# Kernel optimization log

Hardware: AMD Instinct MI355X
Metric: run time of the kernel (lower is better)

## Reference

```python
import jax, jax.numpy as jnp
import numpy as np

N_QUBITS = 4
DEPTH = 3
OUT_DIM = 256
BN_EPS = 1e-5


def _apply_ry(state, theta, q):
    # state: (B,2,2,2,2) complex64, theta: (B,) float32, gate on qubit q
    st = jnp.moveaxis(state, q + 1, -1)            # (B,2,2,2,2) with target last
    half = theta * 0.5
    c = jnp.cos(half)[:, None, None, None]
    s = jnp.sin(half)[:, None, None, None]
    a0, a1 = st[..., 0], st[..., 1]
    st = jnp.stack([c * a0 - s * a1, s * a0 + c * a1], axis=-1)
    return jnp.moveaxis(st, -1, q + 1)


def _apply_rz(state, theta, q):
    # theta: scalar (shared param). RZ = diag(e^{-i t/2}, e^{i t/2})
    st = jnp.moveaxis(state, q + 1, -1)
    p0 = jnp.exp(-0.5j * theta)
    p1 = jnp.exp(0.5j * theta)
    st = jnp.stack([st[..., 0] * p0, st[..., 1] * p1], axis=-1)
    return jnp.moveaxis(st, -1, q + 1)


def _apply_cnot(state, c, t):
    st = jnp.moveaxis(state, (c + 1, t + 1), (-2, -1))  # (...,2_c,2_t)
    st = jnp.stack([st[..., 0, :], st[..., 1, ::-1]], axis=-2)
    return jnp.moveaxis(st, (-2, -1), (c + 1, t + 1))


def _simulate(qparams, x):
    # Batched 4-qubit statevector sim. x: (B,4) data angles, qparams: (24,)
    B = x.shape[0]
    state = jnp.zeros((B, 16), jnp.complex64).at[:, 0].set(1.0)
    state = state.reshape(B, 2, 2, 2, 2)
    for d in range(DEPTH):
        for i in range(N_QUBITS):
            # RY(data) then RY(param) on same wire == RY(data+param)
            state = _apply_ry(state, x[:, i] + qparams[d * 2 * N_QUBITS + i], i)
        for i in range(N_QUBITS):
            state = _apply_cnot(state, i, (i + 1) % N_QUBITS)
        for i in range(N_QUBITS):
            theta = qparams[d * 2 * N_QUBITS + N_QUBITS + i]
            state = _apply_rz(state, jnp.broadcast_to(theta, ()), i)
    probs = jnp.abs(state) ** 2                      # (B,2,2,2,2) float32
    axes = (1, 2, 3, 4)
    z = []
    for i in range(N_QUBITS):
        p = probs.sum(axis=tuple(a for a in axes if a != i + 1))  # (B,2)
        z.append(p[:, 0] - p[:, 1])
    return jnp.stack(z, axis=1).astype(jnp.float32)  # (B,4) <Z_i>


def _batchnorm(h, g, b):
    m = h.mean(axis=0)
    v = h.var(axis=0)  # biased, as torch uses for normalization in train mode
    return (h - m) * jax.lax.rsqrt(v + BN_EPS) * g + b


def setup_inputs() -> dict:
    key = jax.random.key(0)
    ks = jax.random.split(key, 8)
    B = 65536
    x = jax.random.normal(ks[0], (B, N_QUBITS), jnp.float32)
    qparams = jax.random.normal(ks[1], (DEPTH * 2 * N_QUBITS,), jnp.float32)
    fc1_w = jax.random.normal(ks[2], (128, N_QUBITS), jnp.float32) * 0.3
    fc1_b = jnp.zeros((128,), jnp.float32)
    fc2_w = jax.random.normal(ks[3], (256, 128), jnp.float32) * 0.08
    fc2_b = jnp.zeros((256,), jnp.float32)
    fc3_w = jax.random.normal(ks[4], (OUT_DIM, 256), jnp.float32) * 0.06
    fc3_b = jnp.zeros((OUT_DIM,), jnp.float32)
    bn1_g = jnp.ones((128,), jnp.float32)
    bn1_b = jnp.zeros((128,), jnp.float32)
    bn2_g = jnp.ones((256,), jnp.float32)
    bn2_b = jnp.zeros((256,), jnp.float32)
    return dict(x=x, qparams=qparams, fc1_w=fc1_w, fc1_b=fc1_b,
                bn1_g=bn1_g, bn1_b=bn1_b, fc2_w=fc2_w, fc2_b=fc2_b,
                bn2_g=bn2_g, bn2_b=bn2_b, fc3_w=fc3_w, fc3_b=fc3_b)


def reference(x, qparams, fc1_w, fc1_b, bn1_g, bn1_b, fc2_w, fc2_b,
              bn2_g, bn2_b, fc3_w, fc3_b):
    q = _simulate(qparams, x)                              # (B,4)
    h = jax.nn.relu(_batchnorm(q @ fc1_w.T + fc1_b, bn1_g, bn1_b))
    h = jax.nn.relu(_batchnorm(h @ fc2_w.T + fc2_b, bn2_g, bn2_b))
    out = jnp.tanh(h @ fc3_w.T + fc3_b)                    # (B,256)
    return out.reshape(-1, 1, 16, 16)
```

## Files before the change

### kernel.cpp

```cpp
#include <hip/hip_runtime.h>

typedef __attribute__((ext_vector_type(8))) _Float16 f16x8;
typedef __attribute__((ext_vector_type(16))) float f32x16;

#define MFMA32(a, b, c) __builtin_amdgcn_mfma_f32_32x32x16_f16((a), (b), (c), 0, 0, 0)

__device__ __forceinline__ float tanh_fast(float x) {
  return 1.0f - 2.0f / (__expf(2.0f * x) + 1.0f);
}

__global__ __launch_bounds__(256) void k_quantum(
    const float4* __restrict__ x, const float* __restrict__ qp,
    float4* __restrict__ qout, float* __restrict__ stats, int QB,
    const float* __restrict__ w2, const float* __restrict__ w3,
    _Float16* __restrict__ w2f, _Float16* __restrict__ w3f)
{
  int tid = threadIdx.x;

  if (blockIdx.x >= QB) {
    int i = (blockIdx.x - QB) * 256 + tid;
    w3f[i] = (_Float16)w3[i];
    if (i < 32768) w2f[i] = (_Float16)w2[i];
    return;
  }

  size_t r = (size_t)blockIdx.x * 256 + tid;
  float4 xr = x[r];
  float xv[4] = {xr.x, xr.y, xr.z, xr.w};

  float re[16], im[16];
#pragma unroll
  for (int i = 0; i < 16; i++) { re[i] = 0.f; im[i] = 0.f; }
  re[0] = 1.f;

#pragma unroll
  for (int d = 0; d < 3; d++) {
#pragma unroll
    for (int q = 0; q < 4; q++) {
      float th = 0.5f * (xv[q] + qp[d * 8 + q]);
      float s, c; __sincosf(th, &s, &c);
      int m = 8 >> q;
#pragma unroll
      for (int i = 0; i < 16; i++) if (!(i & m)) {
        int i1 = i | m;
        float r0 = re[i], i0 = im[i], r1 = re[i1], i1v = im[i1];
        re[i]  = c * r0 - s * r1;  im[i]  = c * i0 - s * i1v;
        re[i1] = s * r0 + c * r1;  im[i1] = s * i0 + c * i1v;
      }
    }
#pragma unroll
    for (int q = 0; q < 4; q++) {
      int mc = 8 >> q, mt = 8 >> ((q + 1) & 3);
#pragma unroll
      for (int i = 0; i < 16; i++) if ((i & mc) && !(i & mt)) {
        int i1 = i | mt;
        float tr = re[i]; re[i] = re[i1]; re[i1] = tr;
        float ti = im[i]; im[i] = im[i1]; im[i1] = ti;
      }
    }
#pragma unroll
    for (int q = 0; q < 4; q++) {
      float th = 0.5f * qp[d * 8 + 4 + q];
      float s, c; __sincosf(th, &s, &c);
      int m = 8 >> q;
#pragma unroll
      for (int i = 0; i < 16; i++) {
        float pi = (i & m) ? s : -s;
        float r0 = re[i], i0 = im[i];
        re[i] = r0 * c - i0 * pi;
        im[i] = r0 * pi + i0 * c;
      }
    }
  }

  float p[16];
#pragma unroll
  for (int i = 0; i < 16; i++) p[i] = re[i] * re[i] + im[i] * im[i];
  float z[4];
#pragma unroll
  for (int q = 0; q < 4; q++) {
    int m = 8 >> q; float acc = 0.f;
#pragma unroll
    for (int i = 0; i < 16; i++) acc += (i & m) ? -p[i] : p[i];
    z[q] = acc;
  }
  qout[r] = make_float4(z[0], z[1], z[2], z[3]);

  float st[14];
  st[0] = z[0]; st[1] = z[1]; st[2] = z[2]; st[3] = z[3];
  int p5 = 4;
#pragma unroll
  for (int a = 0; a < 4; a++)
#pragma unroll
    for (int b = a; b < 4; b++) st[p5++] = z[a] * z[b];

  __shared__ float part[4][14];
  int lane = tid & 63, wv = tid >> 6;
#pragma unroll
  for (int s = 0; s < 14; s++) {
    float v = st[s];
#pragma unroll
    for (int o = 32; o; o >>= 1) v += __shfl_down(v, o, 64);
    if (lane == 0) part[wv][s] = v;
  }
  __syncthreads();
  if (tid < 14)
    atomicAdd(stats + tid, part[0][tid] + part[1][tid] + part[2][tid] + part[3][tid]);
}

__global__ void k_prep1(const float* __restrict__ w1, const float* __restrict__ b1,
                        const float* __restrict__ g, const float* __restrict__ bb,
                        const float* __restrict__ stats, float* __restrict__ w1e,
                        float* __restrict__ b1e, float invB)
{
  int j = threadIdx.x;
  float qb0 = stats[0] * invB, qb1 = stats[1] * invB, qb2 = stats[2] * invB, qb3 = stats[3] * invB;
  float M00 = stats[4] * invB, M01 = stats[5] * invB, M02 = stats[6] * invB, M03 = stats[7] * invB;
  float M11 = stats[8] * invB, M12 = stats[9] * invB, M13 = stats[10] * invB;
  float M22 = stats[11] * invB, M23 = stats[12] * invB, M33 = stats[13] * invB;
  float w0 = w1[j * 4 + 0], wv1 = w1[j * 4 + 1], wv2 = w1[j * 4 + 2], wv3 = w1[j * 4 + 3];
  float b = b1[j];
  float wq = w0 * qb0 + wv1 * qb1 + wv2 * qb2 + wv3 * qb3;
  float m = wq + b;
  float quad = w0 * w0 * M00 + wv1 * wv1 * M11 + wv2 * wv2 * M22 + wv3 * wv3 * M33
             + 2.f * (w0 * wv1 * M01 + w0 * wv2 * M02 + w0 * wv3 * M03
                    + wv1 * wv2 * M12 + wv1 * wv3 * M13 + wv2 * wv3 * M23);
  float e2 = quad + 2.f * b * wq + b * b;
  float var = e2 - m * m;
  float s = g[j] * rsqrtf(var + 1e-5f);
  w1e[j * 4 + 0] = s * w0; w1e[j * 4 + 1] = s * wv1;
  w1e[j * 4 + 2] = s * wv2; w1e[j * 4 + 3] = s * wv3;
  b1e[j] = s * b + bb[j] - s * m;
}

__global__ __launch_bounds__(256, 2) void k_fc2stats(
    const float4* __restrict__ q, const float4* __restrict__ w1e4,
    const float* __restrict__ b1e, const _Float16* __restrict__ w2f,
    const float* __restrict__ b2,
    float* __restrict__ s2sum, float* __restrict__ s2sq)
{
  __shared__ __align__(16) float4 qs[128];
  __shared__ __align__(16) _Float16 a1[128 * 136];

  int t = threadIdx.x;
  int lane = t & 63, w = t >> 6, m32 = lane & 31, hh = lane >> 5;
  size_t rowBase = (size_t)blockIdx.x * 128;

  if (t < 128) qs[t] = q[rowBase + t];
  __syncthreads();

  {
    int j = t & 127;
    float4 w1 = w1e4[j];
    float b1v = b1e[j];
    int rb = (t >> 7) * 64;
#pragma unroll 8
    for (int i = 0; i < 64; i++) {
      float4 qv = qs[rb + i];
      float v = fmaf(w1.x, qv.x, fmaf(w1.y, qv.y, fmaf(w1.z, qv.z, fmaf(w1.w, qv.w, b1v))));
      a1[(rb + i) * 136 + j] = (_Float16)fmaxf(v, 0.f);
    }
  }
  __syncthreads();

  f32x16 acc[4][2];
#pragma unroll
  for (int mt = 0; mt < 4; mt++)
#pragma unroll
    for (int nt = 0; nt < 2; nt++)
#pragma unroll
      for (int r = 0; r < 16; r++) acc[mt][nt][r] = 0.f;

#pragma unroll
  for (int ks = 0; ks < 8; ks++) {
    int kb = ks * 16 + hh * 8;
    f16x8 bfr[2];
#pragma unroll
    for (int nt = 0; nt < 2; nt++)
      bfr[nt] = *(const f16x8*)(w2f + (size_t)(w * 64 + nt * 32 + m32) * 128 + kb);
#pragma unroll
    for (int mt = 0; mt < 4; mt++) {
      f16x8 afr = *(const f16x8*)&a1[(mt * 32 + m32) * 136 + kb];
#pragma unroll
      for (int nt = 0; nt < 2; nt++)
        acc[mt][nt] = MFMA32(afr, bfr[nt], acc[mt][nt]);
    }
  }

#pragma unroll
  for (int nt = 0; nt < 2; nt++) {
    int col = w * 64 + nt * 32 + m32;
    float b2v = b2[col];
    float s = 0.f, ss = 0.f;
#pragma unroll
    for (int mt = 0; mt < 4; mt++)
#pragma unroll
      for (int r = 0; r < 16; r++) {
        float hv = acc[mt][nt][r] + b2v;
        s += hv; ss += hv * hv;
      }
    s += __shfl_down(s, 32, 64);
    ss += __shfl_down(ss, 32, 64);
    if (lane < 32) {
      atomicAdd(&s2sum[col], s);
      atomicAdd(&s2sq[col], ss);
    }
  }
}

__global__ void k_prep2(const float* __restrict__ g, const float* __restrict__ bb,
                        const float* __restrict__ b2,
                        const float* __restrict__ s2sum, const float* __restrict__ s2sq,
                        float* __restrict__ sc2, float* __restrict__ t2, float invB)
{
  int j = threadIdx.x;
  float m = s2sum[j] * invB;
  float v = s2sq[j] * invB - m * m;
  float s = g[j] * rsqrtf(v + 1e-5f);
  sc2[j] = s;
  t2[j] = bb[j] - m * s + b2[j] * s;
}

__global__ __launch_bounds__(256, 2) void k_final(
    const float4* __restrict__ q, const float4* __restrict__ w1e4,
    const float* __restrict__ b1e, const _Float16* __restrict__ w2f,
    const float* __restrict__ sc2, const float* __restrict__ t2g,
    const _Float16* __restrict__ w3f, const float* __restrict__ b3,
    float* __restrict__ out)
{
  __shared__ __align__(16) float4 qs[128];
  __shared__ __align__(16) _Float16 un[128 * 264];
  _Float16* a1 = un;
  _Float16* a2 = un;

  int t = threadIdx.x;
  int lane = t & 63, w = t >> 6, m32 = lane & 31, hh = lane >> 5;
  size_t rowBase = (size_t)blockIdx.x * 128;

  if (t < 128) qs[t] = q[rowBase + t];
  __syncthreads();

  {
    int j = t & 127;
    float4 w1 = w1e4[j];
    float b1v = b1e[j];
    int rb = (t >> 7) * 64;
#pragma unroll 8
    for (int i = 0; i < 64; i++) {
      float4 qv = qs[rb + i];
      float v = fmaf(w1.x, qv.x, fmaf(w1.y, qv.y, fmaf(w1.z, qv.z, fmaf(w1.w, qv.w, b1v))));
      a1[(rb + i) * 136 + j] = (_Float16)fmaxf(v, 0.f);
    }
  }
  __syncthreads();

  f32x16 acc[4][2];
#pragma unroll
  for (int mt = 0; mt < 4; mt++)
#pragma unroll
    for (int nt = 0; nt < 2; nt++)
#pragma unroll
      for (int r = 0; r < 16; r++) acc[mt][nt][r] = 0.f;

#pragma unroll
  for (int ks = 0; ks < 8; ks++) {
    int kb = ks * 16 + hh * 8;
    f16x8 bfr[2];
#pragma unroll
    for (int nt = 0; nt < 2; nt++)
      bfr[nt] = *(const f16x8*)(w2f + (size_t)(w * 64 + nt * 32 + m32) * 128 + kb);
#pragma unroll
    for (int mt = 0; mt < 4; mt++) {
      f16x8 afr = *(const f16x8*)&a1[(mt * 32 + m32) * 136 + kb];
#pragma unroll
      for (int nt = 0; nt < 2; nt++)
        acc[mt][nt] = MFMA32(afr, bfr[nt], acc[mt][nt]);
    }
  }
  __syncthreads();

#pragma unroll
  for (int nt = 0; nt < 2; nt++) {
    int col = w * 64 + nt * 32 + m32;
    float sv = sc2[col], tv = t2g[col];
#pragma unroll
    for (int mt = 0; mt < 4; mt++)
#pragma unroll
      for (int r = 0; r < 16; r++) {
        int row = mt * 32 + (r & 3) + 8 * (r >> 2) + 4 * hh;
        a2[row * 264 + col] = (_Float16)fmaxf(fmaf(acc[mt][nt][r], sv, tv), 0.f);
      }
  }
  __syncthreads();

  f32x16 acc3[4][2];
#pragma unroll
  for (int mt = 0; mt < 4; mt++)
#pragma unroll
    for (int nt = 0; nt < 2; nt++)
#pragma unroll
      for (int r = 0; r < 16; r++) acc3[mt][nt][r] = 0.f;

#pragma unroll
  for (int ks = 0; ks < 16; ks++) {
    int kb = ks * 16 + hh * 8;
    f16x8 bfr[2];
#pragma unroll
    for (int nt = 0; nt < 2; nt++)
      bfr[nt] = *(const f16x8*)(w3f + (size_t)(w * 64 + nt * 32 + m32) * 256 + kb);
#pragma unroll
    for (int mt = 0; mt < 4; mt++) {
      f16x8 afr = *(const f16x8*)&a2[(mt * 32 + m32) * 264 + kb];
#pragma unroll
      for (int nt = 0; nt < 2; nt++)
        acc3[mt][nt] = MFMA32(afr, bfr[nt], acc3[mt][nt]);
    }
  }

#pragma unroll
  for (int nt = 0; nt < 2; nt++) {
    int col = w * 64 + nt * 32 + m32;
    float b3v = b3[col];
#pragma unroll
    for (int mt = 0; mt < 4; mt++)
#pragma unroll
      for (int r = 0; r < 16; r++) {
        int row = mt * 32 + (r & 3) + 8 * (r >> 2) + 4 * hh;
        out[(rowBase + row) * 256 + col] = tanh_fast(acc3[mt][nt][r] + b3v);
      }
  }
}

extern "C" void kernel_launch(void* const* d_in, const int* in_sizes, int n_in,
                              void* d_out, int out_size, void* d_ws, size_t ws_size,
                              hipStream_t stream) {
  const float* x     = (const float*)d_in[0];
  const float* qp    = (const float*)d_in[1];
  const float* fc1_w = (const float*)d_in[2];
  const float* fc1_b = (const float*)d_in[3];
  const float* bn1_g = (const float*)d_in[4];
  const float* bn1_b = (const float*)d_in[5];
  const float* fc2_w = (const float*)d_in[6];
  const float* fc2_b = (const float*)d_in[7];
  const float* bn2_g = (const float*)d_in[8];
  const float* bn2_b = (const float*)d_in[9];
  const float* fc3_w = (const float*)d_in[10];
  const float* fc3_b = (const float*)d_in[11];
  float* out = (float*)d_out;
  float* ws  = (float*)d_ws;

  int B = in_sizes[0] / 4;
  int QB = B / 256;

  float* wq    = ws;
  float* s1    = ws + (size_t)4 * B;
  float* w1e   = s1 + 16;
  float* b1e   = w1e + 512;
  float* s2sum = b1e + 128;
  float* s2sq  = s2sum + 256;
  float* sc2   = s2sq + 256;
  float* t2    = sc2 + 256;
  _Float16* w2f = (_Float16*)(t2 + 256);
  _Float16* w3f = w2f + 32768;

  hipMemsetAsync((void*)s1, 0, (16 + 512 + 128 + 256 + 256) * sizeof(float), stream);

  float invB = 1.0f / (float)B;

  k_quantum<<<QB + 256, 256, 0, stream>>>((const float4*)x, qp, (float4*)wq, s1, QB,
                                          fc2_w, fc3_w, w2f, w3f);
  k_prep1<<<1, 128, 0, stream>>>(fc1_w, fc1_b, bn1_g, bn1_b, s1, w1e, b1e, invB);
  k_fc2stats<<<B / 128, 256, 0, stream>>>((const float4*)wq, (const float4*)w1e, b1e,
                                          w2f, fc2_b, s2sum, s2sq);
  k_prep2<<<1, 256, 0, stream>>>(bn2_g, bn2_b, fc2_b, s2sum, s2sq, sc2, t2, invB);
  k_final<<<B / 128, 256, 0, stream>>>((const float4*)wq, (const float4*)w1e, b1e,
                                       w2f, sc2, t2, w3f, fc3_b, out);
}
```

Baseline: 149.0 us.

## Store fc2 activations in fp16 and skip recomputing fc1/fc2 in final kernel

```diff
diff --git a/kernel.cpp b/kernel.cpp
--- a/kernel.cpp
+++ b/kernel.cpp
@@ -133,14 +133,16 @@
   b1e[j] = s * b + bb[j] - s * m;
 }
 
-__global__ __launch_bounds__(256, 2) void k_fc2stats(
+__global__ __launch_bounds__(256, 2) void k_fc2h(
     const float4* __restrict__ q, const float4* __restrict__ w1e4,
     const float* __restrict__ b1e, const _Float16* __restrict__ w2f,
-    const float* __restrict__ b2,
+    const float* __restrict__ b2, _Float16* __restrict__ h2f,
     float* __restrict__ s2sum, float* __restrict__ s2sq)
 {
   __shared__ __align__(16) float4 qs[128];
-  __shared__ __align__(16) _Float16 a1[128 * 136];
+  __shared__ __align__(16) _Float16 un[128 * 260];
+  _Float16* a1 = un;
+  _Float16* h2 = un;
 
   int t = threadIdx.x;
   int lane = t & 63, w = t >> 6, m32 = lane & 31, hh = lane >> 5;
@@ -158,7 +160,7 @@
     for (int i = 0; i < 64; i++) {
       float4 qv = qs[rb + i];
       float v = fmaf(w1.x, qv.x, fmaf(w1.y, qv.y, fmaf(w1.z, qv.z, fmaf(w1.w, qv.w, b1v))));
-      a1[(rb + i) * 136 + j] = (_Float16)fmaxf(v, 0.f);
+      a1[(rb + i) * 132 + j] = (_Float16)fmaxf(v, 0.f);
     }
   }
   __syncthreads();
@@ -180,7 +182,7 @@
       bfr[nt] = *(const f16x8*)(w2f + (size_t)(w * 64 + nt * 32 + m32) * 128 + kb);
 #pragma unroll
     for (int mt = 0; mt < 4; mt++) {
-      f16x8 afr = *(const f16x8*)&a1[(mt * 32 + m32) * 136 + kb];
+      f16x8 afr = *(const f16x8*)&a1[(mt * 32 + m32) * 132 + kb];
 #pragma unroll
       for (int nt = 0; nt < 2; nt++)
         acc[mt][nt] = MFMA32(afr, bfr[nt], acc[mt][nt]);
@@ -206,114 +208,83 @@
       atomicAdd(&s2sq[col], ss);
     }
   }
+  __syncthreads();
+
+#pragma unroll
+  for (int nt = 0; nt < 2; nt++) {
+    int col = w * 64 + nt * 32 + m32;
+#pragma unroll
+    for (int mt = 0; mt < 4; mt++)
+#pragma unroll
+      for (int r = 0; r < 16; r++) {
+        int row = mt * 32 + (r & 3) + 8 * (r >> 2) + 4 * hh;
+        h2[row * 260 + col] = (_Float16)acc[mt][nt][r];
+      }
+  }
+  __syncthreads();
+
+  {
+#pragma unroll
+    for (int i = 0; i < 16; i++) {
+      int idx8 = i * 256 + t;
+      int row = idx8 >> 5;
+      int cik = idx8 & 31;
+      *(uint4*)(h2f + (rowBase + row) * 256 + cik * 8) =
+          *(const uint4*)(h2 + row * 260 + cik * 8);
+    }
+  }
 }
 
 __global__ void k_prep2(const float* __restrict__ g, const float* __restrict__ bb,
                         const float* __restrict__ b2,
                         const float* __restrict__ s2sum, const float* __restrict__ s2sq,
-                        float* __restrict__ sc2, float* __restrict__ t2, float invB)
+                        _Float16* __restrict__ sc2h, _Float16* __restrict__ t2h, float invB)
 {
   int j = threadIdx.x;
   float m = s2sum[j] * invB;
   float v = s2sq[j] * invB - m * m;
   float s = g[j] * rsqrtf(v + 1e-5f);
-  sc2[j] = s;
-  t2[j] = bb[j] - m * s + b2[j] * s;
-}
-
-__global__ __launch_bounds__(256, 2) void k_final(
-    const float4* __restrict__ q, const float4* __restrict__ w1e4,
-    const float* __restrict__ b1e, const _Float16* __restrict__ w2f,
-    const float* __restrict__ sc2, const float* __restrict__ t2g,
+  sc2h[j] = (_Float16)s;
+  t2h[j] = (_Float16)(bb[j] - m * s + b2[j] * s);
+}
+
+__global__ __launch_bounds__(256) void k_fc3(
+    const _Float16* __restrict__ h2f,
+    const _Float16* __restrict__ sc2h, const _Float16* __restrict__ t2h,
     const _Float16* __restrict__ w3f, const float* __restrict__ b3,
     float* __restrict__ out)
 {
-  __shared__ __align__(16) float4 qs[128];
-  __shared__ __align__(16) _Float16 un[128 * 264];
-  _Float16* a1 = un;
-  _Float16* a2 = un;
-
   int t = threadIdx.x;
   int lane = t & 63, w = t >> 6, m32 = lane & 31, hh = lane >> 5;
   size_t rowBase = (size_t)blockIdx.x * 128;
 
-  if (t < 128) qs[t] = q[rowBase + t];
-  __syncthreads();
-
-  {
-    int j = t & 127;
-    float4 w1 = w1e4[j];
-    float b1v = b1e[j];
-    int rb = (t >> 7) * 64;
-#pragma unroll 8
-    for (int i = 0; i < 64; i++) {
-      float4 qv = qs[rb + i];
-      float v = fmaf(w1.x, qv.x, fmaf(w1.y, qv.y, fmaf(w1.z, qv.z, fmaf(w1.w, qv.w, b1v))));
-      a1[(rb + i) * 136 + j] = (_Float16)fmaxf(v, 0.f);
-    }
-  }
-  __syncthreads();
-
-  f32x16 acc[4][2];
+  f32x16 acc3[4][2];
 #pragma unroll
   for (int mt = 0; mt < 4; mt++)
 #pragma unroll
     for (int nt = 0; nt < 2; nt++)
 #pragma unroll
-      for (int r = 0; r < 16; r++) acc[mt][nt][r] = 0.f;
-
-#pragma unroll
-  for (int ks = 0; ks < 8; ks++) {
-    int kb = ks * 16 + hh * 8;
-    f16x8 bfr[2];
-#pragma unroll
-    for (int nt = 0; nt < 2; nt++)
-      bfr[nt] = *(const f16x8*)(w2f + (size_t)(w * 64 + nt * 32 + m32) * 128 + kb);
-#pragma unroll
-    for (int mt = 0; mt < 4; mt++) {
-      f16x8 afr = *(const f16x8*)&a1[(mt * 32 + m32) * 136 + kb];
-#pragma unroll
-      for (int nt = 0; nt < 2; nt++)
-        acc[mt][nt] = MFMA32(afr, bfr[nt], acc[mt][nt]);
-    }
-  }
-  __syncthreads();
-
-#pragma unroll
-  for (int nt = 0; nt < 2; nt++) {
-    int col = w * 64 + nt * 32 + m32;
-    float sv = sc2[col], tv = t2g[col];
-#pragma unroll
-    for (int mt = 0; mt < 4; mt++)
-#pragma unroll
-      for (int r = 0; r < 16; r++) {
-        int row = mt * 32 + (r & 3) + 8 * (r >> 2) + 4 * hh;
-        a2[row * 264 + col] = (_Float16)fmaxf(fmaf(acc[mt][nt][r], sv, tv), 0.f);
-      }
-  }
-  __syncthreads();
-
-  f32x16 acc3[4][2];
-#pragma unroll
-  for (int mt = 0; mt < 4; mt++)
-#pragma unroll
-    for (int nt = 0; nt < 2; nt++)
-#pragma unroll
       for (int r = 0; r < 16; r++) acc3[mt][nt][r] = 0.f;
 
-#pragma unroll
+#pragma unroll 4
   for (int ks = 0; ks < 16; ks++) {
     int kb = ks * 16 + hh * 8;
+    f16x8 sv8 = *(const f16x8*)(sc2h + kb);
+    f16x8 tv8 = *(const f16x8*)(t2h + kb);
     f16x8 bfr[2];
 #pragma unroll
     for (int nt = 0; nt < 2; nt++)
       bfr[nt] = *(const f16x8*)(w3f + (size_t)(w * 64 + nt * 32 + m32) * 256 + kb);
 #pragma unroll
     for (int mt = 0; mt < 4; mt++) {
-      f16x8 afr = *(const f16x8*)&a2[(mt * 32 + m32) * 264 + kb];
+      f16x8 hraw = *(const f16x8*)(h2f + (rowBase + mt * 32 + m32) * 256 + kb);
+      f16x8 af = hraw * sv8 + tv8;
+#pragma unroll
+      for (int j = 0; j < 8; j++)
+        af[j] = (af[j] > (_Float16)0.f) ? af[j] : (_Float16)0.f;
 #pragma unroll
       for (int nt = 0; nt < 2; nt++)
-        acc3[mt][nt] = MFMA32(afr, bfr[nt], acc3[mt][nt]);
+        acc3[mt][nt] = MFMA32(af, bfr[nt], acc3[mt][nt]);
     }
   }
 
@@ -358,10 +329,11 @@
   float* b1e   = w1e + 512;
   float* s2sum = b1e + 128;
   float* s2sq  = s2sum + 256;
-  float* sc2   = s2sq + 256;
-  float* t2    = sc2 + 256;
-  _Float16* w2f = (_Float16*)(t2 + 256);
-  _Float16* w3f = w2f + 32768;
+  _Float16* sc2h = (_Float16*)(s2sq + 256);
+  _Float16* t2h  = sc2h + 256;
+  _Float16* w2f  = t2h + 256;
+  _Float16* w3f  = w2f + 32768;
+  _Float16* h2f  = w3f + 65536;
 
   hipMemsetAsync((void*)s1, 0, (16 + 512 + 128 + 256 + 256) * sizeof(float), stream);
 
@@ -370,9 +342,8 @@
   k_quantum<<<QB + 256, 256, 0, stream>>>((const float4*)x, qp, (float4*)wq, s1, QB,
                                           fc2_w, fc3_w, w2f, w3f);
   k_prep1<<<1, 128, 0, stream>>>(fc1_w, fc1_b, bn1_g, bn1_b, s1, w1e, b1e, invB);
-  k_fc2stats<<<B / 128, 256, 0, stream>>>((const float4*)wq, (const float4*)w1e, b1e,
-                                          w2f, fc2_b, s2sum, s2sq);
-  k_prep2<<<1, 256, 0, stream>>>(bn2_g, bn2_b, fc2_b, s2sum, s2sq, sc2, t2, invB);
-  k_final<<<B / 128, 256, 0, stream>>>((const float4*)wq, (const float4*)w1e, b1e,
-                                       w2f, sc2, t2, w3f, fc3_b, out);
-}
+  k_fc2h<<<B / 128, 256, 0, stream>>>((const float4*)wq, (const float4*)w1e, b1e,
+                                      w2f, fc2_b, h2f, s2sum, s2sq);
+  k_prep2<<<1, 256, 0, stream>>>(bn2_g, bn2_b, fc2_b, s2sum, s2sq, sc2h, t2h, invB);
+  k_fc3<<<B / 128, 256, 0, stream>>>(h2f, sc2h, t2h, w3f, fc3_b, out);
+}
```

New measurement: 183.1 us. +22.9%, slower.

## Halve row tile to 64, pre-block fp16 weights for coalesced loads, shrink memset

Applied to the files above, without the earlier changes.

```diff
diff --git a/kernel.cpp b/kernel.cpp
--- a/kernel.cpp
+++ b/kernel.cpp
@@ -13,14 +13,20 @@
     const float4* __restrict__ x, const float* __restrict__ qp,
     float4* __restrict__ qout, float* __restrict__ stats, int QB,
     const float* __restrict__ w2, const float* __restrict__ w3,
-    _Float16* __restrict__ w2f, _Float16* __restrict__ w3f)
+    _Float16* __restrict__ w2t, _Float16* __restrict__ w3t)
 {
   int tid = threadIdx.x;
 
   if (blockIdx.x >= QB) {
     int i = (blockIdx.x - QB) * 256 + tid;
-    w3f[i] = (_Float16)w3[i];
-    if (i < 32768) w2f[i] = (_Float16)w2[i];
+    {
+      int col = i >> 8, k = i & 255;
+      w3t[((k >> 3) * 256 + col) * 8 + (k & 7)] = (_Float16)w3[i];
+    }
+    if (i < 32768) {
+      int col = i >> 7, k = i & 127;
+      w2t[((k >> 3) * 256 + col) * 8 + (k & 7)] = (_Float16)w2[i];
+    }
     return;
   }
 
@@ -133,39 +139,39 @@
   b1e[j] = s * b + bb[j] - s * m;
 }
 
-__global__ __launch_bounds__(256, 2) void k_fc2stats(
+__global__ __launch_bounds__(256, 4) void k_fc2stats(
     const float4* __restrict__ q, const float4* __restrict__ w1e4,
-    const float* __restrict__ b1e, const _Float16* __restrict__ w2f,
+    const float* __restrict__ b1e, const _Float16* __restrict__ w2t,
     const float* __restrict__ b2,
     float* __restrict__ s2sum, float* __restrict__ s2sq)
 {
-  __shared__ __align__(16) float4 qs[128];
-  __shared__ __align__(16) _Float16 a1[128 * 136];
+  __shared__ __align__(16) float4 qs[64];
+  __shared__ __align__(16) _Float16 a1[64 * 132];
 
   int t = threadIdx.x;
   int lane = t & 63, w = t >> 6, m32 = lane & 31, hh = lane >> 5;
-  size_t rowBase = (size_t)blockIdx.x * 128;
-
-  if (t < 128) qs[t] = q[rowBase + t];
+  size_t rowBase = (size_t)blockIdx.x * 64;
+
+  if (t < 64) qs[t] = q[rowBase + t];
   __syncthreads();
 
   {
     int j = t & 127;
     float4 w1 = w1e4[j];
     float b1v = b1e[j];
-    int rb = (t >> 7) * 64;
+    int rb = (t >> 7) * 32;
 #pragma unroll 8
-    for (int i = 0; i < 64; i++) {
+    for (int i = 0; i < 32; i++) {
       float4 qv = qs[rb + i];
       float v = fmaf(w1.x, qv.x, fmaf(w1.y, qv.y, fmaf(w1.z, qv.z, fmaf(w1.w, qv.w, b1v))));
-      a1[(rb + i) * 136 + j] = (_Float16)fmaxf(v, 0.f);
-    }
-  }
-  __syncthreads();
-
-  f32x16 acc[4][2];
-#pragma unroll
-  for (int mt = 0; mt < 4; mt++)
+      a1[(rb + i) * 132 + j] = (_Float16)fmaxf(v, 0.f);
+    }
+  }
+  __syncthreads();
+
+  f32x16 acc[2][2];
+#pragma unroll
+  for (int mt = 0; mt < 2; mt++)
 #pragma unroll
     for (int nt = 0; nt < 2; nt++)
 #pragma unroll
@@ -174,13 +180,14 @@
 #pragma unroll
   for (int ks = 0; ks < 8; ks++) {
     int kb = ks * 16 + hh * 8;
+    int kblock = ks * 2 + hh;
     f16x8 bfr[2];
 #pragma unroll
     for (int nt = 0; nt < 2; nt++)
-      bfr[nt] = *(const f16x8*)(w2f + (size_t)(w * 64 + nt * 32 + m32) * 128 + kb);
-#pragma unroll
-    for (int mt = 0; mt < 4; mt++) {
-      f16x8 afr = *(const f16x8*)&a1[(mt * 32 + m32) * 136 + kb];
+      bfr[nt] = *(const f16x8*)(w2t + (size_t)(kblock * 256 + w * 64 + nt * 32 + m32) * 8);
+#pragma unroll
+    for (int mt = 0; mt < 2; mt++) {
+      f16x8 afr = *(const f16x8*)&a1[(mt * 32 + m32) * 132 + kb];
 #pragma unroll
       for (int nt = 0; nt < 2; nt++)
         acc[mt][nt] = MFMA32(afr, bfr[nt], acc[mt][nt]);
@@ -193,7 +200,7 @@
     float b2v = b2[col];
     float s = 0.f, ss = 0.f;
 #pragma unroll
-    for (int mt = 0; mt < 4; mt++)
+    for (int mt = 0; mt < 2; mt++)
 #pragma unroll
       for (int r = 0; r < 16; r++) {
         float hv = acc[mt][nt][r] + b2v;
@@ -221,42 +228,42 @@
   t2[j] = bb[j] - m * s + b2[j] * s;
 }
 
-__global__ __launch_bounds__(256, 2) void k_final(
+__global__ __launch_bounds__(256, 4) void k_final(
     const float4* __restrict__ q, const float4* __restrict__ w1e4,
-    const float* __restrict__ b1e, const _Float16* __restrict__ w2f,
+    const float* __restrict__ b1e, const _Float16* __restrict__ w2t,
     const float* __restrict__ sc2, const float* __restrict__ t2g,
-    const _Float16* __restrict__ w3f, const float* __restrict__ b3,
+    const _Float16* __restrict__ w3t, const float* __restrict__ b3,
     float* __restrict__ out)
 {
-  __shared__ __align__(16) float4 qs[128];
-  __shared__ __align__(16) _Float16 un[128 * 264];
+  __shared__ __align__(16) float4 qs[64];
+  __shared__ __align__(16) _Float16 un[64 * 260];
   _Float16* a1 = un;
   _Float16* a2 = un;
 
   int t = threadIdx.x;
   int lane = t & 63, w = t >> 6, m32 = lane & 31, hh = lane >> 5;
-  size_t rowBase = (size_t)blockIdx.x * 128;
-
-  if (t < 128) qs[t] = q[rowBase + t];
+  size_t rowBase = (size_t)blockIdx.x * 64;
+
+  if (t < 64) qs[t] = q[rowBase + t];
   __syncthreads();
 
   {
     int j = t & 127;
     float4 w1 = w1e4[j];
     float b1v = b1e[j];
-    int rb = (t >> 7) * 64;
+    int rb = (t >> 7) * 32;
 #pragma unroll 8
-    for (int i = 0; i < 64; i++) {
+    for (int i = 0; i < 32; i++) {
       float4 qv = qs[rb + i];
       float v = fmaf(w1.x, qv.x, fmaf(w1.y, qv.y, fmaf(w1.z, qv.z, fmaf(w1.w, qv.w, b1v))));
-      a1[(rb + i) * 136 + j] = (_Float16)fmaxf(v, 0.f);
-    }
-  }
-  __syncthreads();
-
-  f32x16 acc[4][2];
-#pragma unroll
-  for (int mt = 0; mt < 4; mt++)
+      a1[(rb + i) * 132 + j] = (_Float16)fmaxf(v, 0.f);
+    }
+  }
+  __syncthreads();
+
+  f32x16 acc[2][2];
+#pragma unroll
+  for (int mt = 0; mt < 2; mt++)
 #pragma unroll
     for (int nt = 0; nt < 2; nt++)
 #pragma unroll
@@ -265,52 +272,61 @@
 #pragma unroll
   for (int ks = 0; ks < 8; ks++) {
     int kb = ks * 16 + hh * 8;
+    int kblock = ks * 2 + hh;
     f16x8 bfr[2];
 #pragma unroll
     for (int nt = 0; nt < 2; nt++)
-      bfr[nt] = *(const f16x8*)(w2f + (size_t)(w * 64 + nt * 32 + m32) * 128 + kb);
-#pragma unroll
-    for (int mt = 0; mt < 4; mt++) {
-      f16x8 afr = *(const f16x8*)&a1[(mt * 32 + m32) * 136 + kb];
+      bfr[nt] = *(const f16x8*)(w2t + (size_t)(kblock * 256 + w * 64 + nt * 32 + m32) * 8);
+#pragma unroll
+    for (int mt = 0; mt < 2; mt++) {
+      f16x8 afr = *(const f16x8*)&a1[(mt * 32 + m32) * 132 + kb];
 #pragma unroll
       for (int nt = 0; nt < 2; nt++)
         acc[mt][nt] = MFMA32(afr, bfr[nt], acc[mt][nt]);
     }
   }
-  __syncthreads();
-
+
+  float sv[2], tv[2];
 #pragma unroll
   for (int nt = 0; nt < 2; nt++) {
     int col = w * 64 + nt * 32 + m32;
-    float sv = sc2[col], tv = t2g[col];
-#pragma unroll
-    for (int mt = 0; mt < 4; mt++)
+    sv[nt] = sc2[col];
+    tv[nt] = t2g[col];
+  }
+  __syncthreads();
+
+#pragma unroll
+  for (int nt = 0; nt < 2; nt++) {
+    int col = w * 64 + nt * 32 + m32;
+#pragma unroll
+    for (int mt = 0; mt < 2; mt++)
 #pragma unroll
       for (int r = 0; r < 16; r++) {
         int row = mt * 32 + (r & 3) + 8 * (r >> 2) + 4 * hh;
-        a2[row * 264 + col] = (_Float16)fmaxf(fmaf(acc[mt][nt][r], sv, tv), 0.f);
-      }
-  }
-  __syncthreads();
-
-  f32x16 acc3[4][2];
-#pragma unroll
-  for (int mt = 0; mt < 4; mt++)
+        a2[row * 260 + col] = (_Float16)fmaxf(fmaf(acc[mt][nt][r], sv[nt], tv[nt]), 0.f);
+      }
+  }
+  __syncthreads();
+
+  f32x16 acc3[2][2];
+#pragma unroll
+  for (int mt = 0; mt < 2; mt++)
 #pragma unroll
     for (int nt = 0; nt < 2; nt++)
 #pragma unroll
       for (int r = 0; r < 16; r++) acc3[mt][nt][r] = 0.f;
 
-#pragma unroll
+#pragma unroll 4
   for (int ks = 0; ks < 16; ks++) {
     int kb = ks * 16 + hh * 8;
+    int kblock = ks * 2 + hh;
     f16x8 bfr[2];
 #pragma unroll
     for (int nt = 0; nt < 2; nt++)
-      bfr[nt] = *(const f16x8*)(w3f + (size_t)(w * 64 + nt * 32 + m32) * 256 + kb);
-#pragma unroll
-    for (int mt = 0; mt < 4; mt++) {
-      f16x8 afr = *(const f16x8*)&a2[(mt * 32 + m32) * 264 + kb];
+      bfr[nt] = *(const f16x8*)(w3t + (size_t)(kblock * 256 + w * 64 + nt * 32 + m32) * 8);
+#pragma unroll
+    for (int mt = 0; mt < 2; mt++) {
+      f16x8 afr = *(const f16x8*)&a2[(mt * 32 + m32) * 260 + kb];
 #pragma unroll
       for (int nt = 0; nt < 2; nt++)
         acc3[mt][nt] = MFMA32(afr, bfr[nt], acc3[mt][nt]);
@@ -322,7 +338,7 @@
     int col = w * 64 + nt * 32 + m32;
     float b3v = b3[col];
 #pragma unroll
-    for (int mt = 0; mt < 4; mt++)
+    for (int mt = 0; mt < 2; mt++)
 #pragma unroll
       for (int r = 0; r < 16; r++) {
         int row = mt * 32 + (r & 3) + 8 * (r >> 2) + 4 * hh;
@@ -354,25 +370,25 @@
 
   float* wq    = ws;
   float* s1    = ws + (size_t)4 * B;
-  float* w1e   = s1 + 16;
+  float* s2sum = s1 + 16;
+  float* s2sq  = s2sum + 256;
+  float* w1e   = s2sq + 256;
   float* b1e   = w1e + 512;
-  float* s2sum = b1e + 128;
-  float* s2sq  = s2sum + 256;
-  float* sc2   = s2sq + 256;
+  float* sc2   = b1e + 128;
   float* t2    = sc2 + 256;
-  _Float16* w2f = (_Float16*)(t2 + 256);
-  _Float16* w3f = w2f + 32768;
-
-  hipMemsetAsync((void*)s1, 0, (16 + 512 + 128 + 256 + 256) * sizeof(float), stream);
+  _Float16* w2t = (_Float16*)(t2 + 256);
+  _Float16* w3t = w2t + 32768;
+
+  hipMemsetAsync((void*)s1, 0, (16 + 256 + 256) * sizeof(float), stream);
 
   float invB = 1.0f / (float)B;
 
   k_quantum<<<QB + 256, 256, 0, stream>>>((const float4*)x, qp, (float4*)wq, s1, QB,
-                                          fc2_w, fc3_w, w2f, w3f);
+                                          fc2_w, fc3_w, w2t, w3t);
   k_prep1<<<1, 128, 0, stream>>>(fc1_w, fc1_b, bn1_g, bn1_b, s1, w1e, b1e, invB);
-  k_fc2stats<<<B / 128, 256, 0, stream>>>((const float4*)wq, (const float4*)w1e, b1e,
-                                          w2f, fc2_b, s2sum, s2sq);
+  k_fc2stats<<<B / 64, 256, 0, stream>>>((const float4*)wq, (const float4*)w1e, b1e,
+                                         w2t, fc2_b, s2sum, s2sq);
   k_prep2<<<1, 256, 0, stream>>>(bn2_g, bn2_b, fc2_b, s2sum, s2sq, sc2, t2, invB);
-  k_final<<<B / 128, 256, 0, stream>>>((const float4*)wq, (const float4*)w1e, b1e,
-                                       w2f, sc2, t2, w3f, fc3_b, out);
-}
+  k_final<<<B / 64, 256, 0, stream>>>((const float4*)wq, (const float4*)w1e, b1e,
+                                      w2t, sc2, t2, w3t, fc3_b, out);
+}
```

After: 168.8 us. +13.2%, slower.
